# Kernel optimization log

Hardware: AMD Instinct MI355X
Metric: run time of the kernel (lower is better)

Reference implementation:

```python
import jax, jax.numpy as jnp
import numpy as np

HEADS = 8
DIM_HEAD = 64


def setup_inputs() -> dict:
    key = jax.random.key(0)
    ks = jax.random.split(key, 7)
    b, c, h, w = 8, 256, 64, 64
    hidden = HEADS * DIM_HEAD  # 512
    return {
        "x": jax.random.normal(ks[0], (b, c, h, w), dtype=jnp.float32),
        "context": jax.random.normal(ks[1], (b, c, h, w), dtype=jnp.float32),
        "Wq": jax.random.normal(ks[2], (hidden, c), dtype=jnp.float32) * 0.02,
        "Wk": jax.random.normal(ks[3], (hidden, c), dtype=jnp.float32) * 0.02,
        "Wv": jax.random.normal(ks[4], (hidden, c), dtype=jnp.float32) * 0.02,
        "Wo": jax.random.normal(ks[5], (c, hidden), dtype=jnp.float32) * 0.02,
        "bo": jnp.zeros((c,), dtype=jnp.float32),
    }


def reference(x, context, Wq, Wk, Wv, Wo, bo):
    b, c, h, w = x.shape
    n = h * w
    scale = DIM_HEAD ** (-0.5)
    xf = x.reshape(b, c, n)                      # b c n
    cf = context.reshape(b, context.shape[1], -1)  # b c m
    # 1x1 convs == per-pixel linear projections
    q = jnp.einsum('bcn,oc->bon', xf, Wq).reshape(b, HEADS, DIM_HEAD, n) * scale
    k = jnp.einsum('bcm,oc->bom', cf, Wk).reshape(b, HEADS, DIM_HEAD, -1)
    v = jnp.einsum('bcm,oc->bom', cf, Wv).reshape(b, HEADS, DIM_HEAD, -1)
    k = jax.nn.softmax(k, axis=-1)               # softmax over spatial positions
    ctx = jnp.einsum('bhdm,bhem->bhde', k, v)    # small d x e context
    out = jnp.einsum('bhde,bhdn->bhen', ctx, q)  # b h e n
    out = out.reshape(b, HEADS * DIM_HEAD, h, w)
    return jnp.einsum('bchw,oc->bohw', out, Wo) + bo[None, :, None, None]
```

## Files before the change

kernel.cpp:

```cpp
#include <hip/hip_runtime.h>

#define B   8
#define C   256
#define N   4096
#define H   8
#define D   64
#define HID 512
#define SCALE 0.125f

typedef __attribute__((ext_vector_type(8))) __bf16 bf16x8;
typedef __attribute__((ext_vector_type(4))) float f32x4;

__device__ __forceinline__ ushort f2bf(float f) {
  union { float f; unsigned u; } v; v.f = f;
  unsigned r = v.u + 0x7FFFu + ((v.u >> 16) & 1u);
  return (ushort)(r >> 16);
}

__device__ __forceinline__ f32x4 mfma16(bf16x8 a, bf16x8 b, f32x4 c) {
  return __builtin_amdgcn_mfma_f32_16x16x32_bf16(a, b, c, 0, 0, 0);
}

__device__ __forceinline__ void glds16(const ushort* g, ushort* l) {
  __builtin_amdgcn_global_load_lds(
      (const __attribute__((address_space(1))) void*)g,
      (__attribute__((address_space(3))) void*)l, 16, 0, 0);
}

__global__ __launch_bounds__(256) void prep_kernel(
    const float* __restrict__ x, const float* __restrict__ ctxt,
    const float* __restrict__ Wk, const float* __restrict__ Wv,
    ushort* __restrict__ x_bf, ushort* __restrict__ ctxt_bf,
    ushort* __restrict__ wk_bf, ushort* __restrict__ wv_bf) {
  const int z = blockIdx.z;
  const int tid = threadIdx.x;
  if (z == 16) {
    const int id = blockIdx.y * 64 + blockIdx.x;
    if (id >= 128) return;
    const int t = (id * 256 + tid) * 4;
    const float4 a = *(const float4*)(Wk + t);
    const float4 b = *(const float4*)(Wv + t);
    ushort4 ra, rb;
    ra.x = f2bf(a.x); ra.y = f2bf(a.y); ra.z = f2bf(a.z); ra.w = f2bf(a.w);
    rb.x = f2bf(b.x); rb.y = f2bf(b.y); rb.z = f2bf(b.z); rb.w = f2bf(b.w);
    *(ushort4*)(wk_bf + t) = ra;
    *(ushort4*)(wv_bf + t) = rb;
    return;
  }
  __shared__ float tile[64 * 65];
  const int b = z & 7;
  const float* src = (z < 8) ? ctxt : x;
  ushort* dst = (z < 8) ? ctxt_bf : x_bf;
  const int l0 = blockIdx.x * 64, r0 = blockIdx.y * 64;
  const int rr = tid >> 4, c4 = (tid & 15) << 2;
  const float* sp = src + ((size_t)b * C + r0) * N + l0;
#pragma unroll
  for (int p = 0; p < 4; ++p) {
    const float4 v = *(const float4*)(sp + (size_t)(rr + p * 16) * N + c4);
    float* tp = tile + (rr + p * 16) * 65 + c4;
    tp[0] = v.x; tp[1] = v.y; tp[2] = v.z; tp[3] = v.w;
  }
  __syncthreads();
  const int lr = tid >> 2, rb = (tid & 3) << 4;
  uint pk[8];
#pragma unroll
  for (int k = 0; k < 16; k += 2) {
    const uint lo = f2bf(tile[(rb + k) * 65 + lr]);
    const uint hi = f2bf(tile[(rb + k + 1) * 65 + lr]);
    pk[k >> 1] = lo | (hi << 16);
  }
  ushort* dp = dst + ((size_t)b * N + l0 + lr) * C + r0 + rb;
  *(uint4*)dp = *(uint4*)pk;
  *(uint4*)(dp + 8) = *(uint4*)(pk + 4);
}

__global__ __launch_bounds__(256, 4) void kv_mfma_kernel(
    const ushort* __restrict__ ctxt_bf,
    const ushort* __restrict__ wk_bf,
    const ushort* __restrict__ wv_bf,
    float* __restrict__ ctx_part,
    float* __restrict__ z_part)
{
  __shared__ __align__(16) ushort cb_s[2][32 * 256];
  __shared__ __align__(16) ushort p_s[64 * 32];
  __shared__ __align__(16) ushort v_s[64 * 32];
  const int mt = blockIdx.x, h = blockIdx.y, b = blockIdx.z;
  const int tid = threadIdx.x;
  const int w = tid >> 6, lane = tid & 63;
  const int col = lane & 15, quad = lane >> 4;
  const int dw = w * 16;
  const int swc = (col & 3) ^ ((col >> 2) & 3);

  const ushort* wkp = wk_bf + (size_t)(h * 64 + dw + col) * C + quad * 8;
  const ushort* wvp = wv_bf + (size_t)(h * 64 + dw + col) * C + quad * 8;
  const ushort* cbase = ctxt_bf + ((size_t)b * N + (size_t)mt * 256) * C;

  const int grow0 = w * 8 + (lane >> 5);
  const int ggran = lane & 31;

  const f32x4 z4 = {0.f, 0.f, 0.f, 0.f};
  f32x4 cacc[4];
#pragma unroll
  for (int j = 0; j < 4; ++j) cacc[j] = z4;
  float zl = 0.f;

#pragma unroll
  for (int it = 0; it < 4; ++it) {
    const int row = grow0 + it * 2;
    glds16(cbase + (size_t)row * C + ((ggran ^ (row & 7)) << 3),
           &cb_s[0][(w * 8 + it * 2) * 256]);
  }
  __syncthreads();

  for (int t = 0; t < 8; ++t) {
    const int cur = t & 1;
    if (t < 7) {
      const ushort* nb = cbase + (size_t)(t + 1) * 32 * C;
#pragma unroll
      for (int it = 0; it < 4; ++it) {
        const int row = grow0 + it * 2;
        glds16(nb + (size_t)row * C + ((ggran ^ (row & 7)) << 3),
               &cb_s[cur ^ 1][(w * 8 + it * 2) * 256]);
      }
    }

    f32x4 kacc[2], vacc[2];
#pragma unroll
    for (int i = 0; i < 2; ++i) { kacc[i] = z4; vacc[i] = z4; }
#pragma unroll
    for (int kk = 0; kk < 8; ++kk) {
      bf16x8 a[2];
#pragma unroll
      for (int i = 0; i < 2; ++i) {
        const int r = i * 16 + col;
        a[i] = *(const bf16x8*)(&cb_s[cur][r * 256 +
                  ((((kk << 2) + quad) ^ (r & 7)) << 3)]);
      }
      const bf16x8 wkf = *(const bf16x8*)(wkp + (size_t)kk * 32);
      const bf16x8 wvf = *(const bf16x8*)(wvp + (size_t)kk * 32);
#pragma unroll
      for (int i = 0; i < 2; ++i) {
        kacc[i] = mfma16(a[i], wkf, kacc[i]);
        vacc[i] = mfma16(a[i], wvf, vacc[i]);
      }
    }

#pragma unroll
    for (int i = 0; i < 2; ++i) {
      const int off = (dw + col) * 32 +
                      (((i * 2 + (quad >> 1)) ^ swc) << 3) + ((quad & 1) << 2);
      const f32x4 k4 = kacc[i];
      const float e0 = __expf(k4[0]), e1 = __expf(k4[1]);
      const float e2 = __expf(k4[2]), e3 = __expf(k4[3]);
      zl += (e0 + e1) + (e2 + e3);
      ushort4 pk; pk.x = f2bf(e0); pk.y = f2bf(e1);
      pk.z = f2bf(e2); pk.w = f2bf(e3);
      *(ushort4*)(p_s + off) = pk;
      const f32x4 v4 = vacc[i];
      ushort4 vk; vk.x = f2bf(v4[0]); vk.y = f2bf(v4[1]);
      vk.z = f2bf(v4[2]); vk.w = f2bf(v4[3]);
      *(ushort4*)(v_s + off) = vk;
    }
    __syncthreads();

    {
      const int g = (quad ^ swc) << 3;
      const bf16x8 pa = *(const bf16x8*)(p_s + (dw + col) * 32 + g);
      bf16x8 vb[4];
#pragma unroll
      for (int j = 0; j < 4; ++j)
        vb[j] = *(const bf16x8*)(v_s + (j * 16 + col) * 32 + g);
#pragma unroll
      for (int j = 0; j < 4; ++j) cacc[j] = mfma16(pa, vb[j], cacc[j]);
    }
    __syncthreads();
  }

  {
    float s = zl;
    s += __shfl_xor(s, 16); s += __shfl_xor(s, 32);
    if (quad == 0)
      z_part[((size_t)(b * H + h) * 16 + mt) * 64 + dw + col] = s;
  }

  float* outp = ctx_part + ((size_t)(b * H + h) * 16 + mt) * 4096;
#pragma unroll
  for (int j = 0; j < 4; ++j)
#pragma unroll
    for (int r = 0; r < 4; ++r)
      outp[(size_t)(dw + quad * 4 + r) * 64 + j * 16 + col] = cacc[j][r];
}

__global__ __launch_bounds__(256) void a_kernel(
    const float* __restrict__ ctx_part, const float* __restrict__ z_part,
    const float* __restrict__ Wq, float* __restrict__ A)
{
  const int bh = blockIdx.x, cti = blockIdx.y, tid = threadIdx.x;
  const int b = bh >> 3, h = bh & 7;
  const int c0 = cti << 6;
  __shared__ float ct[64 * 65];
  __shared__ float wq[64 * 68];
  __shared__ float zs[64];
  if (tid < 64) {
    float z = 0.f;
#pragma unroll
    for (int p = 0; p < 16; ++p) z += z_part[((size_t)bh * 16 + p) * 64 + tid];
    zs[tid] = SCALE / z;
  }
  __syncthreads();
  const float* cp = ctx_part + (size_t)bh * 16 * 4096;
  for (int r = 0; r < 16; ++r) {
    const int idx = tid + (r << 8);
    float s = 0.f;
#pragma unroll
    for (int p = 0; p < 16; ++p) s += cp[(size_t)p * 4096 + idx];
    ct[(idx & 63) * 65 + (idx >> 6)] = s * zs[idx >> 6];
    wq[(idx >> 6) * 68 + (idx & 63)] =
        Wq[(size_t)(h * 64 + (idx >> 6)) * C + c0 + (idx & 63)];
  }
  __syncthreads();
  const int e = tid & 63, co = tid >> 6;
  float acc[16];
#pragma unroll
  for (int k = 0; k < 16; ++k) acc[k] = 0.f;
  for (int d = 0; d < 64; ++d) {
    const float cv = ct[e * 65 + d];
    const float* wr = wq + d * 68 + co * 16;
#pragma unroll
    for (int k = 0; k < 16; ++k) acc[k] += cv * wr[k];
  }
  float* Ar = A + ((size_t)b * HID + h * 64 + e) * C + c0 + co * 16;
#pragma unroll
  for (int k = 0; k < 16; ++k) Ar[k] = acc[k];
}

__global__ __launch_bounds__(256) void m_kernel(
    const float* __restrict__ A, const float* __restrict__ Wo,
    ushort* __restrict__ M_bf)
{
  const int tile = blockIdx.x, b = blockIdx.y;
  const int o0 = (tile & 7) << 5, c0 = (tile >> 3) << 6;
  const int tid = threadIdx.x, tx = tid & 15, ty = tid >> 4;
  __shared__ float wo_s[64 * 33];
  __shared__ float a_s[64 * 68];
  float acc[2][4] = {{0.f}};
  const int wo_o = tid >> 3, wo_k = (tid & 7) << 3;
  const int a_k = tid >> 2, a_c = (tid & 3) << 4;
  float4 wr0, wr1, ar0, ar1, ar2, ar3;
  {
    const float* wp = Wo + (size_t)(o0 + wo_o) * HID + wo_k;
    wr0 = *(const float4*)wp; wr1 = *(const float4*)(wp + 4);
    const float* ap = A + ((size_t)b * HID + a_k) * C + c0 + a_c;
    ar0 = *(const float4*)ap;       ar1 = *(const float4*)(ap + 4);
    ar2 = *(const float4*)(ap + 8); ar3 = *(const float4*)(ap + 12);
  }
  for (int t = 0; t < 8; ++t) {
    __syncthreads();
    {
      float* wd = wo_s + wo_k * 33 + wo_o;
      wd[0]   = wr0.x; wd[33]  = wr0.y; wd[66]  = wr0.z; wd[99]  = wr0.w;
      wd[132] = wr1.x; wd[165] = wr1.y; wd[198] = wr1.z; wd[231] = wr1.w;
      float* ad = a_s + a_k * 68 + a_c;
      *(float4*)ad = ar0;       *(float4*)(ad + 4) = ar1;
      *(float4*)(ad + 8) = ar2; *(float4*)(ad + 12) = ar3;
    }
    __syncthreads();
    if (t < 7) {
      const int k0 = (t + 1) << 6;
      const float* wp = Wo + (size_t)(o0 + wo_o) * HID + k0 + wo_k;
      wr0 = *(const float4*)wp; wr1 = *(const float4*)(wp + 4);
      const float* ap = A + ((size_t)b * HID + k0 + a_k) * C + c0 + a_c;
      ar0 = *(const float4*)ap;       ar1 = *(const float4*)(ap + 4);
      ar2 = *(const float4*)(ap + 8); ar3 = *(const float4*)(ap + 12);
    }
#pragma unroll
    for (int kc = 0; kc < 64; ++kc) {
      const float2 wv = *(const float2*)(wo_s + kc * 33 + ty * 2);
      const float4 av = *(const float4*)(a_s + kc * 68 + tx * 4);
      acc[0][0] += wv.x * av.x; acc[0][1] += wv.x * av.y;
      acc[0][2] += wv.x * av.z; acc[0][3] += wv.x * av.w;
      acc[1][0] += wv.y * av.x; acc[1][1] += wv.y * av.y;
      acc[1][2] += wv.y * av.z; acc[1][3] += wv.y * av.w;
    }
  }
#pragma unroll
  for (int i = 0; i < 2; ++i) {
    ushort4 r;
    r.x = f2bf(acc[i][0]); r.y = f2bf(acc[i][1]);
    r.z = f2bf(acc[i][2]); r.w = f2bf(acc[i][3]);
    *(ushort4*)(M_bf + ((size_t)b * C + o0 + ty * 2 + i) * C + c0 + tx * 4) = r;
  }
}

__global__ __launch_bounds__(256, 3) void out_mfma_kernel(
    const ushort* __restrict__ M_bf,
    const ushort* __restrict__ x_bf,
    const float* __restrict__ bo, float* __restrict__ out)
{
  __shared__ __align__(16) ushort xs[2][32 * 256];
  const int nt = blockIdx.x;
  const int ot = blockIdx.y;
  const int b  = blockIdx.z;
  const int tid = threadIdx.x;
  const int w = tid >> 6, lane = tid & 63;
  const int col = lane & 15, quad = lane >> 4;
  const int ow = ot * 128 + w * 32;

  const ushort* xbase = x_bf + ((size_t)b * N + (size_t)nt * 128) * C;
  const int grow0 = w * 8 + (lane >> 5);
  const int ggran = lane & 31;

  bf16x8 mf[8][2];
#pragma unroll
  for (int kk = 0; kk < 8; ++kk)
#pragma unroll
    for (int i = 0; i < 2; ++i)
      mf[kk][i] = *(const bf16x8*)(M_bf +
          ((size_t)b * C + ow + i * 16 + col) * C + kk * 32 + quad * 8);

  float bias[2][4];
#pragma unroll
  for (int i = 0; i < 2; ++i)
#pragma unroll
    for (int r = 0; r < 4; ++r)
      bias[i][r] = bo[ow + i * 16 + quad * 4 + r];

#pragma unroll
  for (int it = 0; it < 4; ++it) {
    const int row = grow0 + it * 2;
    glds16(xbase + (size_t)row * C + ((ggran ^ (row & 7)) << 3),
           &xs[0][(w * 8 + it * 2) * 256]);
  }
  __syncthreads();

  for (int t = 0; t < 4; ++t) {
    const int cur = t & 1;
    if (t < 3) {
      const ushort* nb = xbase + (size_t)(t + 1) * 32 * C;
#pragma unroll
      for (int it = 0; it < 4; ++it) {
        const int row = grow0 + it * 2;
        glds16(nb + (size_t)row * C + ((ggran ^ (row & 7)) << 3),
               &xs[cur ^ 1][(w * 8 + it * 2) * 256]);
      }
    }

    const f32x4 z4 = {0.f, 0.f, 0.f, 0.f};
    f32x4 acc[2][2];
#pragma unroll
    for (int i = 0; i < 2; ++i)
#pragma unroll
      for (int j = 0; j < 2; ++j) acc[i][j] = z4;

#pragma unroll
    for (int kk = 0; kk < 8; ++kk) {
      bf16x8 bx[2];
#pragma unroll
      for (int j = 0; j < 2; ++j) {
        const int r = j * 16 + col;
        bx[j] = *(const bf16x8*)(&xs[cur][r * 256 +
                  ((((kk << 2) + quad) ^ (r & 7)) << 3)]);
      }
#pragma unroll
      for (int i = 0; i < 2; ++i)
#pragma unroll
        for (int j = 0; j < 2; ++j)
          acc[i][j] = mfma16(mf[kk][i], bx[j], acc[i][j]);
    }

#pragma unroll
    for (int i = 0; i < 2; ++i)
#pragma unroll
      for (int r = 0; r < 4; ++r) {
        const int o = ow + i * 16 + quad * 4 + r;
        float* op = out + ((size_t)b * C + o) * N + nt * 128 + t * 32 + col;
#pragma unroll
        for (int j = 0; j < 2; ++j)
          op[j * 16] = acc[i][j][r] + bias[i][r];
      }
    __syncthreads();
  }
}

extern "C" void kernel_launch(void* const* d_in, const int* in_sizes, int n_in,
                              void* d_out, int out_size, void* d_ws, size_t ws_size,
                              hipStream_t stream) {
  const float* x    = (const float*)d_in[0];
  const float* ctxt = (const float*)d_in[1];
  const float* Wq   = (const float*)d_in[2];
  const float* Wk   = (const float*)d_in[3];
  const float* Wv   = (const float*)d_in[4];
  const float* Wo   = (const float*)d_in[5];
  const float* bo   = (const float*)d_in[6];
  float* out = (float*)d_out;

  char* p = (char*)d_ws;
  ushort* ctxt_bf = (ushort*)p;  p += (size_t)B * N * C * 2;
  ushort* x_bf    = (ushort*)p;  p += (size_t)B * N * C * 2;
  ushort* wk_bf   = (ushort*)p;  p += (size_t)HID * C * 2;
  ushort* wv_bf   = (ushort*)p;  p += (size_t)HID * C * 2;
  ushort* M_bf    = (ushort*)p;  p += (size_t)B * C * C * 2;
  float*  z_part  = (float*)p;   p += (size_t)B * H * 16 * 64 * 4;
  float*  A       = (float*)p;   p += (size_t)B * HID * C * 4;
  float*  ctx_part= (float*)p;   p += (size_t)B * H * 16 * 4096 * 4;

  prep_kernel<<<dim3(N / 64, C / 64, 17), 256, 0, stream>>>(
      x, ctxt, Wk, Wv, x_bf, ctxt_bf, wk_bf, wv_bf);
  kv_mfma_kernel<<<dim3(16, H, B), 256, 0, stream>>>(
      ctxt_bf, wk_bf, wv_bf, ctx_part, z_part);
  a_kernel<<<dim3(B * H, 4), 256, 0, stream>>>(ctx_part, z_part, Wq, A);
  m_kernel<<<dim3(32, B), 256, 0, stream>>>(A, Wo, M_bf);
  out_mfma_kernel<<<dim3(32, 2, B), 256, 0, stream>>>(M_bf, x_bf, bo, out);
}
```

Before: 190.8 us.

## Move x transpose/convert into a_kernel launch to overlap with small A computation

The x fp32→bf16 transpose is split out of the prep kernel and placed as extra blocks in the a_kernel launch. The small 256-block A computation, which underfills the GPU, now runs alongside 2048 transpose blocks. This is meant to hide the A kernel's low occupancy and shorten the prep kernel on the critical path before kv_mfma. Shared memory is unioned, so the A blocks keep their LDS footprint, and block scheduling order may leave the A blocks waiting behind transpose blocks.

```diff
diff --git a/kernel.cpp b/kernel.cpp
--- a/kernel.cpp
+++ b/kernel.cpp
@@ -28,13 +28,13 @@
 }
 
 __global__ __launch_bounds__(256) void prep_kernel(
-    const float* __restrict__ x, const float* __restrict__ ctxt,
+    const float* __restrict__ ctxt,
     const float* __restrict__ Wk, const float* __restrict__ Wv,
-    ushort* __restrict__ x_bf, ushort* __restrict__ ctxt_bf,
+    ushort* __restrict__ ctxt_bf,
     ushort* __restrict__ wk_bf, ushort* __restrict__ wv_bf) {
   const int z = blockIdx.z;
   const int tid = threadIdx.x;
-  if (z == 16) {
+  if (z == 8) {
     const int id = blockIdx.y * 64 + blockIdx.x;
     if (id >= 128) return;
     const int t = (id * 256 + tid) * 4;
@@ -48,12 +48,10 @@
     return;
   }
   __shared__ float tile[64 * 65];
-  const int b = z & 7;
-  const float* src = (z < 8) ? ctxt : x;
-  ushort* dst = (z < 8) ? ctxt_bf : x_bf;
+  const int b = z;
   const int l0 = blockIdx.x * 64, r0 = blockIdx.y * 64;
   const int rr = tid >> 4, c4 = (tid & 15) << 2;
-  const float* sp = src + ((size_t)b * C + r0) * N + l0;
+  const float* sp = ctxt + ((size_t)b * C + r0) * N + l0;
 #pragma unroll
   for (int p = 0; p < 4; ++p) {
     const float4 v = *(const float4*)(sp + (size_t)(rr + p * 16) * N + c4);
@@ -69,7 +67,7 @@
     const uint hi = f2bf(tile[(rb + k + 1) * 65 + lr]);
     pk[k >> 1] = lo | (hi << 16);
   }
-  ushort* dp = dst + ((size_t)b * N + l0 + lr) * C + r0 + rb;
+  ushort* dp = ctxt_bf + ((size_t)b * N + l0 + lr) * C + r0 + rb;
   *(uint4*)dp = *(uint4*)pk;
   *(uint4*)(dp + 8) = *(uint4*)(pk + 4);
 }
@@ -191,21 +189,53 @@
       outp[(size_t)(dw + quad * 4 + r) * 64 + j * 16 + col] = cacc[j][r];
 }
 
-__global__ __launch_bounds__(256) void a_kernel(
+__global__ __launch_bounds__(256) void a_xpose_kernel(
     const float* __restrict__ ctx_part, const float* __restrict__ z_part,
-    const float* __restrict__ Wq, float* __restrict__ A)
+    const float* __restrict__ Wq, float* __restrict__ A,
+    const float* __restrict__ x, ushort* __restrict__ x_bf)
 {
-  const int bh = blockIdx.x, cti = blockIdx.y, tid = threadIdx.x;
+  __shared__ union {
+    struct { float ct[64 * 65]; float wq[64 * 68]; float zs[64]; } a;
+    float tile[64 * 65];
+  } sm;
+  const int gid = blockIdx.x;
+  const int tid = threadIdx.x;
+
+  if (gid >= 256) {
+    const int t = gid - 256;
+    const int b = t >> 8, rem = t & 255;
+    const int l0 = (rem >> 2) * 64, r0 = (rem & 3) * 64;
+    const int rr = tid >> 4, c4 = (tid & 15) << 2;
+    const float* sp = x + ((size_t)b * C + r0) * N + l0;
+#pragma unroll
+    for (int p = 0; p < 4; ++p) {
+      const float4 v = *(const float4*)(sp + (size_t)(rr + p * 16) * N + c4);
+      float* tp = sm.tile + (rr + p * 16) * 65 + c4;
+      tp[0] = v.x; tp[1] = v.y; tp[2] = v.z; tp[3] = v.w;
+    }
+    __syncthreads();
+    const int lr = tid >> 2, rb = (tid & 3) << 4;
+    uint pk[8];
+#pragma unroll
+    for (int k = 0; k < 16; k += 2) {
+      const uint lo = f2bf(sm.tile[(rb + k) * 65 + lr]);
+      const uint hi = f2bf(sm.tile[(rb + k + 1) * 65 + lr]);
+      pk[k >> 1] = lo | (hi << 16);
+    }
+    ushort* dp = x_bf + ((size_t)b * N + l0 + lr) * C + r0 + rb;
+    *(uint4*)dp = *(uint4*)pk;
+    *(uint4*)(dp + 8) = *(uint4*)(pk + 4);
+    return;
+  }
+
+  const int bh = gid >> 2, cti = gid & 3;
   const int b = bh >> 3, h = bh & 7;
   const int c0 = cti << 6;
-  __shared__ float ct[64 * 65];
-  __shared__ float wq[64 * 68];
-  __shared__ float zs[64];
   if (tid < 64) {
     float z = 0.f;
 #pragma unroll
     for (int p = 0; p < 16; ++p) z += z_part[((size_t)bh * 16 + p) * 64 + tid];
-    zs[tid] = SCALE / z;
+    sm.a.zs[tid] = SCALE / z;
   }
   __syncthreads();
   const float* cp = ctx_part + (size_t)bh * 16 * 4096;
@@ -214,8 +244,8 @@
     float s = 0.f;
 #pragma unroll
     for (int p = 0; p < 16; ++p) s += cp[(size_t)p * 4096 + idx];
-    ct[(idx & 63) * 65 + (idx >> 6)] = s * zs[idx >> 6];
-    wq[(idx >> 6) * 68 + (idx & 63)] =
+    sm.a.ct[(idx & 63) * 65 + (idx >> 6)] = s * sm.a.zs[idx >> 6];
+    sm.a.wq[(idx >> 6) * 68 + (idx & 63)] =
         Wq[(size_t)(h * 64 + (idx >> 6)) * C + c0 + (idx & 63)];
   }
   __syncthreads();
@@ -224,8 +254,8 @@
 #pragma unroll
   for (int k = 0; k < 16; ++k) acc[k] = 0.f;
   for (int d = 0; d < 64; ++d) {
-    const float cv = ct[e * 65 + d];
-    const float* wr = wq + d * 68 + co * 16;
+    const float cv = sm.a.ct[e * 65 + d];
+    const float* wr = sm.a.wq + d * 68 + co * 16;
 #pragma unroll
     for (int k = 0; k < 16; ++k) acc[k] += cv * wr[k];
   }
@@ -404,11 +434,12 @@
   float*  A       = (float*)p;   p += (size_t)B * HID * C * 4;
   float*  ctx_part= (float*)p;   p += (size_t)B * H * 16 * 4096 * 4;
 
-  prep_kernel<<<dim3(N / 64, C / 64, 17), 256, 0, stream>>>(
-      x, ctxt, Wk, Wv, x_bf, ctxt_bf, wk_bf, wv_bf);
+  prep_kernel<<<dim3(N / 64, C / 64, 9), 256, 0, stream>>>(
+      ctxt, Wk, Wv, ctxt_bf, wk_bf, wv_bf);
   kv_mfma_kernel<<<dim3(16, H, B), 256, 0, stream>>>(
       ctxt_bf, wk_bf, wv_bf, ctx_part, z_part);
-  a_kernel<<<dim3(B * H, 4), 256, 0, stream>>>(ctx_part, z_part, Wq, A);
+  a_xpose_kernel<<<dim3(256 + 2048), 256, 0, stream>>>(
+      ctx_part, z_part, Wq, A, x, x_bf);
   m_kernel<<<dim3(32, B), 256, 0, stream>>>(A, Wo, M_bf);
   out_mfma_kernel<<<dim3(32, 2, B), 256, 0, stream>>>(M_bf, x_bf, bo, out);
 }
```

Result: no change. 193.2 us (+1.3%).
